# Kernel optimization log

Measured on AMD Instinct MI355X. Metric: run time of the kernel, lower is better.

The kernel has to match this reference:

```python
import jax, jax.numpy as jnp
import numpy as np

T, B, D, H = 1024, 8, 1024, 16

def setup_inputs() -> dict:
    key = jax.random.key(0)
    ks = jax.random.split(key, 9)
    s = 0.02
    return {
        "x": jax.random.normal(ks[0], (T, B, D), dtype=jnp.float32),
        "Wq": jax.random.normal(ks[1], (D, D), dtype=jnp.float32) * s,
        "bq": jnp.zeros((D,), dtype=jnp.float32),
        "Wk": jax.random.normal(ks[2], (D, D), dtype=jnp.float32) * s,
        "bk": jnp.zeros((D,), dtype=jnp.float32),
        "Wv": jax.random.normal(ks[3], (D, D), dtype=jnp.float32) * s,
        "bv": jnp.zeros((D,), dtype=jnp.float32),
        "Wo": jax.random.normal(ks[4], (D, D), dtype=jnp.float32) * s,
        "bo": jnp.zeros((D,), dtype=jnp.float32),
        "n_heads": H,
    }

def reference(x, Wq, bq, Wk, bk, Wv, bv, Wo, bo, n_heads):
    t, b, D = x.shape
    h = n_heads
    d = D // h
    scale = 1.0 / jnp.sqrt(jnp.float32(d))
    # nn.Linear: y = x @ W.T + b
    q = (x @ Wq.T + bq).reshape(t, b, h, d)
    k = (x @ Wk.T + bk).reshape(t, b, h, d)
    v = (x @ Wv.T + bv).reshape(t, b, h, d)
    # scores: [b, h, t_query, t_key]
    scores = jnp.einsum('tbhd,sbhd->bhts', q, k) * scale
    attn = jax.nn.softmax(scores, axis=-1)
    out = jnp.einsum('bhts,sbhd->tbhd', attn, v).reshape(t, b, D)
    return out @ Wo.T + bo
```

## Files before the change

kernel.cpp:

```cpp
#include <hip/hip_runtime.h>


#define Tn 1024
#define Bn 8
#define Dn 1024
#define Hn 16
#define HDn 64
#define Mn 8192
#define Kn 1024

typedef float f32x4 __attribute__((ext_vector_type(4)));
typedef __bf16 bf16x8 __attribute__((ext_vector_type(8)));
typedef unsigned short u16x8 __attribute__((ext_vector_type(8)));
typedef unsigned short u16x4 __attribute__((ext_vector_type(4)));

#define GLL16(g, l)                                                        \
  __builtin_amdgcn_global_load_lds(                                        \
      (const __attribute__((address_space(1))) void*)(g),                  \
      (__attribute__((address_space(3))) void*)(l), 16, 0, 0)

__device__ __forceinline__ unsigned short f2bf(float f) {
  unsigned int u = __float_as_uint(f);
  u += 0x7fffu + ((u >> 16) & 1u);
  return (unsigned short)(u >> 16);
}

__device__ __forceinline__ unsigned short bfbits(float f) {
  __bf16 h = (__bf16)f;
  return __builtin_bit_cast(unsigned short, h);
}

__global__ __launch_bounds__(256) void cvt_all(
    const float* __restrict__ x, const float* __restrict__ s0,
    const float* __restrict__ s1, const float* __restrict__ s2,
    const float* __restrict__ s3, unsigned short* __restrict__ dx,
    unsigned short* __restrict__ d0, unsigned short* __restrict__ d1,
    unsigned short* __restrict__ d2, unsigned short* __restrict__ d3) {
  const int z = blockIdx.z;
  const float* src;
  unsigned short* dst;
  int n4;
  if (z == 0)      { src = x;  dst = dx; n4 = Mn * Kn / 4; }
  else if (z == 1) { src = s0; dst = d0; n4 = Dn * Dn / 4; }
  else if (z == 2) { src = s1; dst = d1; n4 = Dn * Dn / 4; }
  else if (z == 3) { src = s2; dst = d2; n4 = Dn * Dn / 4; }
  else             { src = s3; dst = d3; n4 = Dn * Dn / 4; }
  int i = blockIdx.x * 256 + threadIdx.x;
  const int stride = gridDim.x * 256;
  for (; i < n4; i += stride) {
    const float4 v = ((const float4*)src)[i];
    u16x4 o;
    o.x = f2bf(v.x); o.y = f2bf(v.y); o.z = f2bf(v.z); o.w = f2bf(v.w);
    ((u16x4*)dst)[i] = o;
  }
}

__device__ __forceinline__ void gemm128_core(
    const unsigned short* __restrict__ A, const unsigned short* __restrict__ Bw,
    unsigned short* lds_a, unsigned short* lds_b,
    int bm, int bn, f32x4 acc[4][4]) {
  const int tid = threadIdx.x;
  const int lane = tid & 63;
  const int w = tid >> 6;
  const int wr = w >> 1, wc = w & 1;
  const int fr = lane & 15, fg = lane >> 4;

  const int p0 = tid, p1 = tid + 256;
  const int r0 = p0 >> 2, c0 = (p0 & 3) ^ ((r0 ^ (r0 >> 2)) & 3);
  const int r1 = p1 >> 2, c1 = (p1 & 3) ^ ((r1 ^ (r1 >> 2)) & 3);
  const unsigned short* gA0 = A + (size_t)(bm * 128 + r0) * Kn + c0 * 8;
  const unsigned short* gA1 = A + (size_t)(bm * 128 + r1) * Kn + c1 * 8;
  const unsigned short* gB0 = Bw + (size_t)(bn * 128 + r0) * Kn + c0 * 8;
  const unsigned short* gB1 = Bw + (size_t)(bn * 128 + r1) * Kn + c1 * 8;

  int aoff[4], boff[4];
#pragma unroll
  for (int m = 0; m < 4; m++) {
    const int row = wr * 64 + m * 16 + fr;
    aoff[m] = row * 32 + ((fg ^ ((row ^ (row >> 2)) & 3)) * 8);
  }
#pragma unroll
  for (int n = 0; n < 4; n++) {
    const int row = wc * 64 + n * 16 + fr;
    boff[n] = row * 32 + ((fg ^ ((row ^ (row >> 2)) & 3)) * 8);
  }

#define GSTAGE(koff, bi)                                                  \
  do {                                                                    \
    GLL16(gA0 + (koff), &lds_a[(bi) * 4096 + tid * 8]);                   \
    GLL16(gA1 + (koff), &lds_a[(bi) * 4096 + (tid + 256) * 8]);           \
    GLL16(gB0 + (koff), &lds_b[(bi) * 4096 + tid * 8]);                   \
    GLL16(gB1 + (koff), &lds_b[(bi) * 4096 + (tid + 256) * 8]);           \
  } while (0)

  GSTAGE(0, 0);
  __syncthreads();

  for (int kk = 0; kk < 32; ++kk) {
    const int cur = kk & 1;
    if (kk < 31) GSTAGE((kk + 1) * 32, cur ^ 1);
    const unsigned short* la = lds_a + cur * 4096;
    const unsigned short* lb = lds_b + cur * 4096;
    bf16x8 af[4], bfr[4];
#pragma unroll
    for (int m = 0; m < 4; m++) af[m] = *(const bf16x8*)&la[aoff[m]];
#pragma unroll
    for (int n = 0; n < 4; n++) bfr[n] = *(const bf16x8*)&lb[boff[n]];
#pragma unroll
    for (int m = 0; m < 4; m++)
#pragma unroll
      for (int n = 0; n < 4; n++)
        acc[m][n] = __builtin_amdgcn_mfma_f32_16x16x32_bf16(af[m], bfr[n],
                                                            acc[m][n], 0, 0, 0);
    __syncthreads();
  }
#undef GSTAGE
}

__global__ __launch_bounds__(256) void gemm_qkv(
    const unsigned short* __restrict__ xbf, const unsigned short* __restrict__ wq,
    const unsigned short* __restrict__ wk, const unsigned short* __restrict__ wv,
    const float* __restrict__ bq, const float* __restrict__ bk,
    const float* __restrict__ bv, unsigned short* __restrict__ qd,
    unsigned short* __restrict__ kd, unsigned short* __restrict__ vd) {
  __shared__ __align__(16) unsigned short lds_a[2 * 128 * 32];
  __shared__ __align__(16) unsigned short lds_b[2 * 128 * 32];
  const int z = blockIdx.z;
  const unsigned short* Bw = (z == 0) ? wq : (z == 1) ? wk : wv;
  const float* bias = (z == 0) ? bq : (z == 1) ? bk : bv;
  unsigned short* dst = (z == 0) ? qd : (z == 1) ? kd : vd;
  const float sc = (z == 0) ? 0.125f * 1.44269504088896f : 1.0f;

  f32x4 acc[4][4] = {};
  gemm128_core(xbf, Bw, lds_a, lds_b, blockIdx.x, blockIdx.y, acc);

  const int tid = threadIdx.x, lane = tid & 63, w = tid >> 6;
  const int wr = w >> 1, wc = w & 1, fr = lane & 15, fg = lane >> 4;
#pragma unroll
  for (int n = 0; n < 4; n++) {
    const int gcol = blockIdx.y * 128 + wc * 64 + n * 16 + fr;
    const float bc = bias[gcol];
    const int hh = gcol >> 6, dd = gcol & 63;
#pragma unroll
    for (int m = 0; m < 4; m++) {
      const int rowbase = blockIdx.x * 128 + wr * 64 + m * 16 + fg * 4;
#pragma unroll
      for (int r = 0; r < 4; r++) {
        const int grow = rowbase + r;
        const int tt = grow >> 3, bb = grow & 7;
        const float v = (acc[m][n][r] + bc) * sc;
        dst[((size_t)(bb * Hn + hh) * Tn + tt) * HDn + dd] = f2bf(v);
      }
    }
  }
}

__global__ __launch_bounds__(256) void gemm_out(
    const unsigned short* __restrict__ abf, const unsigned short* __restrict__ wo,
    const float* __restrict__ bo, float* __restrict__ out) {
  __shared__ __align__(16) unsigned short lds_a[2 * 128 * 32];
  __shared__ __align__(16) unsigned short lds_b[2 * 128 * 32];
  f32x4 acc[4][4] = {};
  gemm128_core(abf, wo, lds_a, lds_b, blockIdx.x, blockIdx.y, acc);

  const int tid = threadIdx.x, lane = tid & 63, w = tid >> 6;
  const int wr = w >> 1, wc = w & 1, fr = lane & 15, fg = lane >> 4;
#pragma unroll
  for (int n = 0; n < 4; n++) {
    const int gcol = blockIdx.y * 128 + wc * 64 + n * 16 + fr;
    const float bc = bo[gcol];
#pragma unroll
    for (int m = 0; m < 4; m++) {
      const int rowbase = blockIdx.x * 128 + wr * 64 + m * 16 + fg * 4;
#pragma unroll
      for (int r = 0; r < 4; r++) {
        const int grow = rowbase + r;
        out[(size_t)grow * Dn + gcol] = acc[m][n][r] + bc;
      }
    }
  }
}

__global__ __launch_bounds__(256) void transpose_v(
    const unsigned short* __restrict__ src, unsigned short* __restrict__ dst) {
  __shared__ unsigned short tile[64][72];
  const int tid = threadIdx.x;
  const size_t base = (size_t)blockIdx.y * ((size_t)Tn * HDn);
  const int t0 = blockIdx.x * 64;
#pragma unroll
  for (int it = 0; it < 2; it++) {
    const int p = it * 256 + tid;
    const int r = p >> 3, c = (p & 7) * 8;
    *(u16x8*)&tile[r][c] =
        *(const u16x8*)(src + base + (size_t)(t0 + r) * HDn + c);
  }
  __syncthreads();
#pragma unroll
  for (int it = 0; it < 2; it++) {
    const int p = it * 256 + tid;
    const int d = p >> 3, tc = (p & 7) * 8;
    u16x8 v;
#pragma unroll
    for (int j = 0; j < 8; j++) v[j] = tile[tc + j][d];
    *(u16x8*)(dst + base + (size_t)d * Tn + t0 + tc) = v;
  }
}

__global__ __launch_bounds__(256) void attn_fwd(
    const unsigned short* __restrict__ Q, const unsigned short* __restrict__ K,
    const unsigned short* __restrict__ Vt, unsigned short* __restrict__ Ob) {
  __shared__ __align__(16) unsigned short k2[2][64 * 64];
  __shared__ __align__(16) unsigned short v2[2][64 * 64];
  __shared__ __align__(16) unsigned short p_all[64 * 64];

  const int tid = threadIdx.x, lane = tid & 63, w = tid >> 6;
  const int fr = lane & 15, fg = lane >> 4;
  const int bh = blockIdx.x;
  const int qt = blockIdx.y;
  const int bb = bh >> 4, hh = bh & 15;

  const unsigned short* Qbh = Q + (size_t)bh * (Tn * HDn);
  const unsigned short* Kbh = K + (size_t)bh * (Tn * HDn);
  const unsigned short* Vbh = Vt + (size_t)bh * (HDn * Tn);

  const int p0 = tid, p1 = tid + 256;
  const int r0 = p0 >> 3, c0 = (p0 & 7) ^ (r0 & 7);
  const int r1 = p1 >> 3, c1 = (p1 & 7) ^ (r1 & 7);

  GLL16(Qbh + (size_t)(qt * 64 + r0) * HDn + c0 * 8, &p_all[p0 * 8]);
  GLL16(Qbh + (size_t)(qt * 64 + r1) * HDn + c1 * 8, &p_all[p1 * 8]);
  __syncthreads();
  bf16x8 qa[2];
#pragma unroll
  for (int ks = 0; ks < 2; ks++) {
    const int row = w * 16 + fr;
    const int blk = (ks * 4 + fg) ^ (row & 7);
    qa[ks] = *(const bf16x8*)&p_all[row * 64 + blk * 8];
  }

  bf16x8 vones;
#pragma unroll
  for (int j = 0; j < 8; j++) vones[j] = (__bf16)1.0f;

#define STAGE_KV(nx, bi)                                                     \
  do {                                                                       \
    GLL16(Kbh + (size_t)((nx) * 64 + r0) * HDn + c0 * 8, &k2[bi][p0 * 8]);   \
    GLL16(Kbh + (size_t)((nx) * 64 + r1) * HDn + c1 * 8, &k2[bi][p1 * 8]);   \
    GLL16(Vbh + (size_t)r0 * Tn + (nx) * 64 + c0 * 8, &v2[bi][p0 * 8]);      \
    GLL16(Vbh + (size_t)r1 * Tn + (nx) * 64 + c1 * 8, &v2[bi][p1 * 8]);      \
  } while (0)

  STAGE_KV(0, 0);
  __syncthreads();

  f32x4 o[4] = {};
  float lsum[4] = {};
  const float FM = 12.0f;

  for (int kt = 0; kt < 16; kt++) {
    const int cur = kt & 1;
    if (kt < 15) STAGE_KV(kt + 1, cur ^ 1);
    const unsigned short* kl = k2[cur];
    const unsigned short* vl = v2[cur];

    f32x4 s[4] = {};
    __builtin_amdgcn_s_setprio(1);
#pragma unroll
    for (int n = 0; n < 4; n++)
#pragma unroll
      for (int ks = 0; ks < 2; ks++) {
        const int krow = n * 16 + fr;
        const int blk = (ks * 4 + fg) ^ (krow & 7);
        const bf16x8 kb = *(const bf16x8*)&kl[krow * 64 + blk * 8];
        s[n] = __builtin_amdgcn_mfma_f32_16x16x32_bf16(kb, qa[ks], s[n], 0, 0, 0);
      }
    __builtin_amdgcn_s_setprio(0);

#pragma unroll
    for (int n = 0; n < 4; n++) {
      u16x4 pk;
#pragma unroll
      for (int r = 0; r < 4; r++) pk[r] = bfbits(exp2f(s[n][r] - FM));
      const int addr = (w * 16 + fr) * 64 +
                       (((2 * n + (fg >> 1)) ^ (fr & 7)) * 8) + (fg & 1) * 4;
      *(u16x4*)&p_all[addr] = pk;
    }

    bf16x8 pa[2];
#pragma unroll
    for (int ks = 0; ks < 2; ks++) {
      const int blk = (ks * 4 + fg) ^ (fr & 7);
      pa[ks] = *(const bf16x8*)&p_all[(w * 16 + fr) * 64 + blk * 8];
    }

    f32x4 ss = {};
    ss = __builtin_amdgcn_mfma_f32_16x16x32_bf16(pa[0], vones, ss, 0, 0, 0);
    ss = __builtin_amdgcn_mfma_f32_16x16x32_bf16(pa[1], vones, ss, 0, 0, 0);
#pragma unroll
    for (int r = 0; r < 4; r++) lsum[r] += ss[r];

    __builtin_amdgcn_s_setprio(1);
#pragma unroll
    for (int ks = 0; ks < 2; ks++)
#pragma unroll
      for (int n = 0; n < 4; n++) {
        const int vrow = n * 16 + fr;
        const int vblk = (ks * 4 + fg) ^ (vrow & 7);
        const bf16x8 vb = *(const bf16x8*)&vl[vrow * 64 + vblk * 8];
        o[n] = __builtin_amdgcn_mfma_f32_16x16x32_bf16(pa[ks], vb, o[n], 0, 0, 0);
      }
    __builtin_amdgcn_s_setprio(0);
    __syncthreads();
  }
#undef STAGE_KV

#pragma unroll
  for (int r = 0; r < 4; r++) lsum[r] = 1.0f / lsum[r];
  const int tbase = qt * 64 + w * 16 + fg * 4;
#pragma unroll
  for (int n = 0; n < 4; n++) {
    const int dcol = n * 16 + fr;
#pragma unroll
    for (int r = 0; r < 4; r++) {
      const int tt = tbase + r;
      const float val = o[n][r] * lsum[r];
      Ob[((size_t)(tt * Bn + bb)) * Dn + hh * HDn + dcol] = bfbits(val);
    }
  }
}

extern "C" void kernel_launch(void* const* d_in, const int* in_sizes, int n_in,
                              void* d_out, int out_size, void* d_ws,
                              size_t ws_size, hipStream_t stream) {
  (void)in_sizes; (void)n_in; (void)out_size; (void)ws_size;
  const float* x  = (const float*)d_in[0];
  const float* Wq = (const float*)d_in[1];
  const float* bq = (const float*)d_in[2];
  const float* Wk = (const float*)d_in[3];
  const float* bk = (const float*)d_in[4];
  const float* Wv = (const float*)d_in[5];
  const float* bv = (const float*)d_in[6];
  const float* Wo = (const float*)d_in[7];
  const float* bo = (const float*)d_in[8];
  float* out = (float*)d_out;

  unsigned short* ws  = (unsigned short*)d_ws;
  unsigned short* xbf = ws;
  unsigned short* wqb = xbf + (size_t)Mn * Kn;
  unsigned short* wkb = wqb + (size_t)Dn * Dn;
  unsigned short* wvb = wkb + (size_t)Dn * Dn;
  unsigned short* wob = wvb + (size_t)Dn * Dn;
  unsigned short* qb  = wob + (size_t)Dn * Dn;
  unsigned short* kb  = qb + (size_t)Mn * Dn;
  unsigned short* vb  = kb + (size_t)Mn * Dn;
  unsigned short* vtb = xbf;
  unsigned short* ab  = vb;

  cvt_all<<<dim3(512, 1, 5), 256, 0, stream>>>(
      x, Wq, Wk, Wv, Wo, xbf, wqb, wkb, wvb, wob);

  gemm_qkv<<<dim3(Mn / 128, Dn / 128, 3), 256, 0, stream>>>(
      xbf, wqb, wkb, wvb, bq, bk, bv, qb, kb, vb);
  transpose_v<<<dim3(Tn / 64, Bn * Hn), 256, 0, stream>>>(vb, vtb);
  attn_fwd<<<dim3(Bn * Hn, Tn / 64), 256, 0, stream>>>(qb, kb, vtb, ab);
  gemm_out<<<dim3(Mn / 128, Dn / 128), 256, 0, stream>>>(ab, wob, bo, out);
}
```

Measured before the change: 290.2 us.

## Use single-buffered BK=64 GEMM tiles and flatten conversion kernel grid

The shared GEMM core moves from a double-buffered K-tile of 32 to a single-buffered K-tile of 64, with a new XOR swizzle over 8 column blocks. Each 64-wide tile is loaded, then a barrier, then two MFMA k-steps, then a barrier. This halves the number of barrier iterations and doubles the MFMA work per barrier, but it loses the overlap of global loads with compute that double buffering gave. The fp32-to-bf16 conversion kernel is also changed from a 5-slice z-grid, where the weight slices were much smaller than the x slice, to one flat 2048-block grid, which balances work across blocks.

Measured after the change: 268.1 us. -7.6%, faster.

```diff
diff --git a/kernel.cpp b/kernel.cpp
--- a/kernel.cpp
+++ b/kernel.cpp
@@ -31,27 +31,33 @@
 }
 
 __global__ __launch_bounds__(256) void cvt_all(
-    const float* __restrict__ x, const float* __restrict__ s0,
-    const float* __restrict__ s1, const float* __restrict__ s2,
-    const float* __restrict__ s3, unsigned short* __restrict__ dx,
+    const float* __restrict__ x, const float* __restrict__ w0,
+    const float* __restrict__ w1, const float* __restrict__ w2,
+    const float* __restrict__ w3, unsigned short* __restrict__ dx,
     unsigned short* __restrict__ d0, unsigned short* __restrict__ d1,
     unsigned short* __restrict__ d2, unsigned short* __restrict__ d3) {
-  const int z = blockIdx.z;
-  const float* src;
-  unsigned short* dst;
-  int n4;
-  if (z == 0)      { src = x;  dst = dx; n4 = Mn * Kn / 4; }
-  else if (z == 1) { src = s0; dst = d0; n4 = Dn * Dn / 4; }
-  else if (z == 2) { src = s1; dst = d1; n4 = Dn * Dn / 4; }
-  else if (z == 3) { src = s2; dst = d2; n4 = Dn * Dn / 4; }
-  else             { src = s3; dst = d3; n4 = Dn * Dn / 4; }
+  const int NX = Mn * Kn / 4;
+  const int NW = Dn * Dn / 4;
+  const int NT = NX + 4 * NW;
   int i = blockIdx.x * 256 + threadIdx.x;
   const int stride = gridDim.x * 256;
-  for (; i < n4; i += stride) {
-    const float4 v = ((const float4*)src)[i];
+  for (; i < NT; i += stride) {
+    const float* src;
+    unsigned short* dst;
+    int j;
+    if (i < NX) {
+      src = x; dst = dx; j = i;
+    } else {
+      const int t = i - NX;
+      const int wsel = t >> 18;
+      j = t & (NW - 1);
+      src = (wsel == 0) ? w0 : (wsel == 1) ? w1 : (wsel == 2) ? w2 : w3;
+      dst = (wsel == 0) ? d0 : (wsel == 1) ? d1 : (wsel == 2) ? d2 : d3;
+    }
+    const float4 v = ((const float4*)src)[j];
     u16x4 o;
     o.x = f2bf(v.x); o.y = f2bf(v.y); o.z = f2bf(v.z); o.w = f2bf(v.w);
-    ((u16x4*)dst)[i] = o;
+    ((u16x4*)dst)[j] = o;
   }
 }
 
@@ -65,56 +71,54 @@
   const int wr = w >> 1, wc = w & 1;
   const int fr = lane & 15, fg = lane >> 4;
 
-  const int p0 = tid, p1 = tid + 256;
-  const int r0 = p0 >> 2, c0 = (p0 & 3) ^ ((r0 ^ (r0 >> 2)) & 3);
-  const int r1 = p1 >> 2, c1 = (p1 & 3) ^ ((r1 ^ (r1 >> 2)) & 3);
-  const unsigned short* gA0 = A + (size_t)(bm * 128 + r0) * Kn + c0 * 8;
-  const unsigned short* gA1 = A + (size_t)(bm * 128 + r1) * Kn + c1 * 8;
-  const unsigned short* gB0 = Bw + (size_t)(bn * 128 + r0) * Kn + c0 * 8;
-  const unsigned short* gB1 = Bw + (size_t)(bn * 128 + r1) * Kn + c1 * 8;
-
-  int aoff[4], boff[4];
+  int goffA[4], goffB[4];
+#pragma unroll
+  for (int i = 0; i < 4; i++) {
+    const int p = tid + 256 * i;
+    const int r = p >> 3, cblk = (p & 7) ^ (r & 7);
+    goffA[i] = (bm * 128 + r) * Kn + cblk * 8;
+    goffB[i] = (bn * 128 + r) * Kn + cblk * 8;
+  }
+  int aoff[4][2], boff[4][2];
 #pragma unroll
   for (int m = 0; m < 4; m++) {
     const int row = wr * 64 + m * 16 + fr;
-    aoff[m] = row * 32 + ((fg ^ ((row ^ (row >> 2)) & 3)) * 8);
+#pragma unroll
+    for (int kk = 0; kk < 2; kk++)
+      aoff[m][kk] = row * 64 + (((kk * 4 + fg) ^ (row & 7)) * 8);
   }
 #pragma unroll
   for (int n = 0; n < 4; n++) {
     const int row = wc * 64 + n * 16 + fr;
-    boff[n] = row * 32 + ((fg ^ ((row ^ (row >> 2)) & 3)) * 8);
-  }
-
-#define GSTAGE(koff, bi)                                                  \
-  do {                                                                    \
-    GLL16(gA0 + (koff), &lds_a[(bi) * 4096 + tid * 8]);                   \
-    GLL16(gA1 + (koff), &lds_a[(bi) * 4096 + (tid + 256) * 8]);           \
-    GLL16(gB0 + (koff), &lds_b[(bi) * 4096 + tid * 8]);                   \
-    GLL16(gB1 + (koff), &lds_b[(bi) * 4096 + (tid + 256) * 8]);           \
-  } while (0)
-
-  GSTAGE(0, 0);
-  __syncthreads();
-
-  for (int kk = 0; kk < 32; ++kk) {
-    const int cur = kk & 1;
-    if (kk < 31) GSTAGE((kk + 1) * 32, cur ^ 1);
-    const unsigned short* la = lds_a + cur * 4096;
-    const unsigned short* lb = lds_b + cur * 4096;
-    bf16x8 af[4], bfr[4];
-#pragma unroll
-    for (int m = 0; m < 4; m++) af[m] = *(const bf16x8*)&la[aoff[m]];
-#pragma unroll
-    for (int n = 0; n < 4; n++) bfr[n] = *(const bf16x8*)&lb[boff[n]];
-#pragma unroll
-    for (int m = 0; m < 4; m++)
-#pragma unroll
-      for (int n = 0; n < 4; n++)
-        acc[m][n] = __builtin_amdgcn_mfma_f32_16x16x32_bf16(af[m], bfr[n],
-                                                            acc[m][n], 0, 0, 0);
+#pragma unroll
+    for (int kk = 0; kk < 2; kk++)
+      boff[n][kk] = row * 64 + (((kk * 4 + fg) ^ (row & 7)) * 8);
+  }
+
+  for (int kt = 0; kt < 16; ++kt) {
+    const int kbase = kt * 64;
+#pragma unroll
+    for (int i = 0; i < 4; i++) {
+      GLL16(A + goffA[i] + kbase, &lds_a[(tid + 256 * i) * 8]);
+      GLL16(Bw + goffB[i] + kbase, &lds_b[(tid + 256 * i) * 8]);
+    }
     __syncthreads();
-  }
-#undef GSTAGE
+#pragma unroll
+    for (int kk = 0; kk < 2; kk++) {
+      bf16x8 af[4], bfr[4];
+#pragma unroll
+      for (int m = 0; m < 4; m++) af[m] = *(const bf16x8*)&lds_a[aoff[m][kk]];
+#pragma unroll
+      for (int n = 0; n < 4; n++) bfr[n] = *(const bf16x8*)&lds_b[boff[n][kk]];
+#pragma unroll
+      for (int m = 0; m < 4; m++)
+#pragma unroll
+        for (int n = 0; n < 4; n++)
+          acc[m][n] = __builtin_amdgcn_mfma_f32_16x16x32_bf16(
+              af[m], bfr[n], acc[m][n], 0, 0, 0);
+    }
+    __syncthreads();
+  }
 }
 
 __global__ __launch_bounds__(256) void gemm_qkv(
@@ -123,8 +127,8 @@
     const float* __restrict__ bq, const float* __restrict__ bk,
     const float* __restrict__ bv, unsigned short* __restrict__ qd,
     unsigned short* __restrict__ kd, unsigned short* __restrict__ vd) {
-  __shared__ __align__(16) unsigned short lds_a[2 * 128 * 32];
-  __shared__ __align__(16) unsigned short lds_b[2 * 128 * 32];
+  __shared__ __align__(16) unsigned short lds_a[128 * 64];
+  __shared__ __align__(16) unsigned short lds_b[128 * 64];
   const int z = blockIdx.z;
   const unsigned short* Bw = (z == 0) ? wq : (z == 1) ? wk : wv;
   const float* bias = (z == 0) ? bq : (z == 1) ? bk : bv;
@@ -158,8 +162,8 @@
 __global__ __launch_bounds__(256) void gemm_out(
     const unsigned short* __restrict__ abf, const unsigned short* __restrict__ wo,
     const float* __restrict__ bo, float* __restrict__ out) {
-  __shared__ __align__(16) unsigned short lds_a[2 * 128 * 32];
-  __shared__ __align__(16) unsigned short lds_b[2 * 128 * 32];
+  __shared__ __align__(16) unsigned short lds_a[128 * 64];
+  __shared__ __align__(16) unsigned short lds_b[128 * 64];
   f32x4 acc[4][4] = {};
   gemm128_core(abf, wo, lds_a, lds_b, blockIdx.x, blockIdx.y, acc);
 
@@ -356,7 +360,7 @@
   unsigned short* vtb = xbf;
   unsigned short* ab  = vb;
 
-  cvt_all<<<dim3(512, 1, 5), 256, 0, stream>>>(
+  cvt_all<<<2048, 256, 0, stream>>>(
       x, Wq, Wk, Wv, Wo, xbf, wqb, wkb, wvb, wob);
 
   gemm_qkv<<<dim3(Mn / 128, Dn / 128, 3), 256, 0, stream>>>(
```
